# Optimization experiments

Hardware: AMD Instinct MI355X
Metric: run time of the kernel (lower is better)

Reference implementation:

```python
import jax, jax.numpy as jnp
import numpy as np
import math

D_MODEL = 256
NUM_HEADS = 8
D_HEAD = 32
K_EIG = 32
NUM_BANDS = 3


def setup_inputs() -> dict:
    key = jax.random.key(0)
    ks = jax.random.split(key, 12)
    B, N = 2, 50000
    x = jax.random.normal(ks[0], (B, N, D_MODEL), dtype=jnp.float32)
    eigenvectors = jax.random.normal(ks[1], (N, K_EIG), dtype=jnp.float32) / np.sqrt(N)
    eigenvalues = jnp.sort(jax.random.uniform(ks[2], (K_EIG,), dtype=jnp.float32))
    s = 1.0 / np.sqrt(D_MODEL)
    Wq = jax.random.normal(ks[3], (NUM_HEADS * D_HEAD, D_MODEL), dtype=jnp.float32) * s
    bq = jnp.zeros((NUM_HEADS * D_HEAD,), dtype=jnp.float32)
    Wk = jax.random.normal(ks[4], (NUM_HEADS * D_HEAD, D_MODEL), dtype=jnp.float32) * s
    bk = jnp.zeros((NUM_HEADS * D_HEAD,), dtype=jnp.float32)
    Wv = jax.random.normal(ks[5], (NUM_HEADS * D_HEAD, D_MODEL), dtype=jnp.float32) * s
    bv = jnp.zeros((NUM_HEADS * D_HEAD,), dtype=jnp.float32)
    # per-head SpectralFilter params
    band_boundaries = jnp.tile(jnp.linspace(0.0, 1.0, NUM_BANDS + 1, dtype=jnp.float32)[None, :], (NUM_HEADS, 1))
    filter_weights = jnp.ones((NUM_HEADS, NUM_BANDS, K_EIG), dtype=jnp.float32) + 0.1 * jax.random.normal(ks[6], (NUM_HEADS, NUM_BANDS, K_EIG), dtype=jnp.float32)
    return {"x": x, "eigenvectors": eigenvectors, "eigenvalues": eigenvalues,
            "Wq": Wq, "bq": bq, "Wk": Wk, "bk": bk, "Wv": Wv, "bv": bv,
            "band_boundaries": band_boundaries, "filter_weights": filter_weights}


def _filter_responses(eigenvalues, band_boundaries, filter_weights):
    # eigenvalues [K]; band_boundaries [H, NB+1]; filter_weights [H, NB, K] -> [H, K]
    lam = (eigenvalues - eigenvalues.min()) / (eigenvalues.max() - eigenvalues.min() + 1e-8)  # [K]
    resp = jnp.zeros(filter_weights.shape[::2], dtype=eigenvalues.dtype)  # [H, K]
    for i in range(NUM_BANDS):  # small fixed loop; later bands overwrite (faithful to torch)
        lo = band_boundaries[:, i:i + 1]   # [H,1]
        hi = band_boundaries[:, i + 1:i + 2]
        mask = (lam[None, :] >= lo) & (lam[None, :] < hi)  # [H,K]
        resp = jnp.where(mask, filter_weights[:, i, :], resp)
    return resp


def reference(x, eigenvectors, eigenvalues, Wq, bq, Wk, bk, Wv, bv, band_boundaries, filter_weights):
    B, N, D = x.shape
    H, Dh = NUM_HEADS, D_HEAD
    Q = (x @ Wq.T + bq).reshape(B, N, H, Dh)
    K = (x @ Wk.T + bk).reshape(B, N, H, Dh)
    V = (x @ Wv.T + bv).reshape(B, N, H, Dh)
    # project to spectral domain: [B,K,H,Dh]
    Qf = jnp.einsum('nk,bnhd->bkhd', eigenvectors, Q)
    Kf = jnp.einsum('nk,bnhd->bkhd', eigenvectors, K)
    Vf = jnp.einsum('nk,bnhd->bkhd', eigenvectors, V)
    resp = _filter_responses(eigenvalues, band_boundaries, filter_weights)  # [H,K]
    g = resp.T[None, :, :, None]  # [1,K,H,1]
    Qf, Kf, Vf = Qf * g, Kf * g, Vf * g
    scores = jnp.einsum('bkhd,blhd->bkhl', Qf, Kf) / math.sqrt(Dh)  # [B,K,H,K]
    attn = jax.nn.softmax(scores, axis=-1)
    out_freq = jnp.einsum('bkhl,blhd->bkhd', attn, Vf)
    out = jnp.einsum('nk,bkhd->bnhd', eigenvectors, out_freq)
    return out.reshape(B, N, H * Dh)
```

## Files before the change

kernel.cpp:

```cpp
#include <hip/hip_runtime.h>
#include <hip/hip_bf16.h>


constexpr int D = 256;

__global__ __launch_bounds__(256) void k_colsum(const float* __restrict__ E,
                                                float* __restrict__ pS, int N) {
  int k = threadIdx.x & 31;
  int rg = threadIdx.x >> 5;
  int rs = (N + 255) >> 8;
  int n0 = blockIdx.x * rs;
  int n1 = n0 + rs; if (n1 > N) n1 = N;
  float acc = 0.f;
  for (int n = n0 + rg; n < n1; n += 8) acc += E[(size_t)n * 32 + k];
  __shared__ float red[256];
  red[threadIdx.x] = acc;
  __syncthreads();
  if (threadIdx.x < 32) {
    float t = red[threadIdx.x];
#pragma unroll
    for (int i = 1; i < 8; ++i) t += red[i * 32 + threadIdx.x];
    pS[blockIdx.x * 32 + threadIdx.x] = t;
  }
}

__global__ __launch_bounds__(256) void k_partial(const float* __restrict__ x,
                                                 const float* __restrict__ E,
                                                 float* __restrict__ pU,
                                                 int N, int nchunk, int rpc) {
  int bc = blockIdx.x;
  int c = bc % nchunk;
  int b = bc / nchunk;
  int t = threadIdx.x;
  int w = t >> 6;
  int lane = t & 63;
  int n0 = c * rpc;
  int n1 = n0 + rpc; if (n1 > N) n1 = N;
  int nrows = n1 - n0; if (nrows < 0) nrows = 0;

  __shared__ __align__(16) float4 xs[2][1024];
  __shared__ __align__(16) float4 es[2][128];

  float4 a0={0,0,0,0}, a1={0,0,0,0}, a2={0,0,0,0}, a3={0,0,0,0};
  float4 a4={0,0,0,0}, a5={0,0,0,0}, a6={0,0,0,0}, a7={0,0,0,0};

  if (nrows > 0) {
    const float4* g4 = reinterpret_cast<const float4*>(x) + (size_t)b * N * 64;
    const float4* e4 = reinterpret_cast<const float4*>(E);
    int xr = t >> 6;
    int xq = t & 63;
    int er = t >> 3;
    int eq = t & 7;

    float4 rx0, rx1, rx2, rx3, re;
#define CL(r) ((r) < N - 1 ? (r) : N - 1)
    {
      rx0 = g4[(size_t)CL(n0 + xr +  0) * 64 + xq];
      rx1 = g4[(size_t)CL(n0 + xr +  4) * 64 + xq];
      rx2 = g4[(size_t)CL(n0 + xr +  8) * 64 + xq];
      rx3 = g4[(size_t)CL(n0 + xr + 12) * 64 + xq];
      if (t < 128) re = e4[(size_t)CL(n0 + er) * 8 + eq];
    }
    int ntiles = (nrows + 15) >> 4;
#pragma unroll 1
    for (int tt = 0; tt < ntiles; ++tt) {
      int buf = tt & 1;
      xs[buf][(xr +  0) * 64 + xq] = rx0;
      xs[buf][(xr +  4) * 64 + xq] = rx1;
      xs[buf][(xr +  8) * 64 + xq] = rx2;
      xs[buf][(xr + 12) * 64 + xq] = rx3;
      if (t < 128) es[buf][t] = re;
      __syncthreads();
      if (tt + 1 < ntiles) {
        int tb = n0 + ((tt + 1) << 4);
        rx0 = g4[(size_t)CL(tb + xr +  0) * 64 + xq];
        rx1 = g4[(size_t)CL(tb + xr +  4) * 64 + xq];
        rx2 = g4[(size_t)CL(tb + xr +  8) * 64 + xq];
        rx3 = g4[(size_t)CL(tb + xr + 12) * 64 + xq];
        if (t < 128) re = e4[(size_t)CL(tb + er) * 8 + eq];
      }
      int tr = nrows - (tt << 4); if (tr > 16) tr = 16;
#pragma unroll 4
      for (int r = 0; r < tr; ++r) {
        float4 xv = xs[buf][r * 64 + lane];
        float4 e0 = es[buf][r * 8 + 2 * w];
        float4 e1 = es[buf][r * 8 + 2 * w + 1];
        a0.x = fmaf(e0.x, xv.x, a0.x); a0.y = fmaf(e0.x, xv.y, a0.y);
        a0.z = fmaf(e0.x, xv.z, a0.z); a0.w = fmaf(e0.x, xv.w, a0.w);
        a1.x = fmaf(e0.y, xv.x, a1.x); a1.y = fmaf(e0.y, xv.y, a1.y);
        a1.z = fmaf(e0.y, xv.z, a1.z); a1.w = fmaf(e0.y, xv.w, a1.w);
        a2.x = fmaf(e0.z, xv.x, a2.x); a2.y = fmaf(e0.z, xv.y, a2.y);
        a2.z = fmaf(e0.z, xv.z, a2.z); a2.w = fmaf(e0.z, xv.w, a2.w);
        a3.x = fmaf(e0.w, xv.x, a3.x); a3.y = fmaf(e0.w, xv.y, a3.y);
        a3.z = fmaf(e0.w, xv.z, a3.z); a3.w = fmaf(e0.w, xv.w, a3.w);
        a4.x = fmaf(e1.x, xv.x, a4.x); a4.y = fmaf(e1.x, xv.y, a4.y);
        a4.z = fmaf(e1.x, xv.z, a4.z); a4.w = fmaf(e1.x, xv.w, a4.w);
        a5.x = fmaf(e1.y, xv.x, a5.x); a5.y = fmaf(e1.y, xv.y, a5.y);
        a5.z = fmaf(e1.y, xv.z, a5.z); a5.w = fmaf(e1.y, xv.w, a5.w);
        a6.x = fmaf(e1.z, xv.x, a6.x); a6.y = fmaf(e1.z, xv.y, a6.y);
        a6.z = fmaf(e1.z, xv.z, a6.z); a6.w = fmaf(e1.z, xv.w, a6.w);
        a7.x = fmaf(e1.w, xv.x, a7.x); a7.y = fmaf(e1.w, xv.y, a7.y);
        a7.z = fmaf(e1.w, xv.z, a7.z); a7.w = fmaf(e1.w, xv.w, a7.w);
      }
      __syncthreads();
    }
#undef CL
  }

  float4* o4 = reinterpret_cast<float4*>(pU) + (size_t)bc * 2048
             + (size_t)(8 * w) * 64 + lane;
  o4[0 * 64] = a0; o4[1 * 64] = a1; o4[2 * 64] = a2; o4[3 * 64] = a3;
  o4[4 * 64] = a4; o4[5 * 64] = a5; o4[6 * 64] = a6; o4[7 * 64] = a7;
}

__global__ __launch_bounds__(256) void k_reduce(const float* __restrict__ pU,
                                                float* __restrict__ U, int nchunk) {
  int e = blockIdx.x * 32 + (threadIdx.x & 31);
  int sub = threadIdx.x >> 5;
  int b = e >> 13;
  int kd = e & 8191;
  const float* p = pU + (size_t)b * nchunk * 8192 + kd;
  float a0 = 0.f, a1 = 0.f, a2 = 0.f, a3 = 0.f;
  float a4 = 0.f, a5 = 0.f, a6 = 0.f, a7 = 0.f;
  int c = sub;
#pragma unroll 1
  for (; c + 56 < nchunk; c += 64) {
    a0 += p[(size_t)c * 8192];
    a1 += p[(size_t)(c + 8) * 8192];
    a2 += p[(size_t)(c + 16) * 8192];
    a3 += p[(size_t)(c + 24) * 8192];
    a4 += p[(size_t)(c + 32) * 8192];
    a5 += p[(size_t)(c + 40) * 8192];
    a6 += p[(size_t)(c + 48) * 8192];
    a7 += p[(size_t)(c + 56) * 8192];
  }
  for (; c < nchunk; c += 8) a0 += p[(size_t)c * 8192];
  __shared__ float red[256];
  red[threadIdx.x] = ((a0 + a1) + (a2 + a3)) + ((a4 + a5) + (a6 + a7));
  __syncthreads();
  if (threadIdx.x < 32) {
    float s = red[threadIdx.x];
#pragma unroll
    for (int i = 1; i < 8; ++i) s += red[i * 32 + threadIdx.x];
    U[e] = s;
  }
}

__global__ __launch_bounds__(256) void k_project(
    const float* __restrict__ U, const float* __restrict__ pS,
    const float* __restrict__ Wq, const float* __restrict__ bq,
    const float* __restrict__ Wk, const float* __restrict__ bk,
    const float* __restrict__ Wv, const float* __restrict__ bv,
    const float* __restrict__ ev, const float* __restrict__ bb,
    const float* __restrict__ fw,
    float* __restrict__ Qfg, float* __restrict__ Kfg, float* __restrict__ Vfg) {
  int blk = blockIdx.x;
  int k = blk & 31;
  int t = threadIdx.x;
  __shared__ __align__(16) float u[256];
  __shared__ float red[256];
  u[t] = U[(size_t)blk * 256 + t];
  red[t] = pS[t * 32 + k];
  __syncthreads();
#pragma unroll
  for (int off = 128; off > 0; off >>= 1) {
    if (t < off) red[t] += red[t + off];
    __syncthreads();
  }
  float sk = red[0];

  float mnf = ev[0], mxf = ev[0];
#pragma unroll
  for (int i = 1; i < 32; ++i) { float v = ev[i]; mnf = fminf(mnf, v); mxf = fmaxf(mxf, v); }
  double mn = (double)mnf, mx = (double)mxf;
  double lam = ((double)ev[k] - mn) / (mx - mn + 1e-8);
  int h = t >> 5;
  float g = 0.f;
#pragma unroll
  for (int i = 0; i < 3; ++i) {
    double lo = (double)bb[h * 4 + i], hi = (double)bb[h * 4 + i + 1];
    if (lam >= lo && lam < hi) g = fw[(h * 3 + i) * 32 + k];
  }

  const float4* u4 = reinterpret_cast<const float4*>(u);
  const float4* wq4 = reinterpret_cast<const float4*>(Wq) + (size_t)t * 64;
  const float4* wk4 = reinterpret_cast<const float4*>(Wk) + (size_t)t * 64;
  const float4* wv4 = reinterpret_cast<const float4*>(Wv) + (size_t)t * 64;
  float aq = 0.f, ak = 0.f, av = 0.f;
#pragma unroll 4
  for (int j = 0; j < 64; ++j) {
    float4 uv = u4[j];
    float4 q = wq4[j], kk = wk4[j], vv = wv4[j];
    aq = fmaf(uv.x, q.x, aq);  aq = fmaf(uv.y, q.y, aq);
    aq = fmaf(uv.z, q.z, aq);  aq = fmaf(uv.w, q.w, aq);
    ak = fmaf(uv.x, kk.x, ak); ak = fmaf(uv.y, kk.y, ak);
    ak = fmaf(uv.z, kk.z, ak); ak = fmaf(uv.w, kk.w, ak);
    av = fmaf(uv.x, vv.x, av); av = fmaf(uv.y, vv.y, av);
    av = fmaf(uv.z, vv.z, av); av = fmaf(uv.w, vv.w, av);
  }
  Qfg[(size_t)blk * 256 + t] = (aq + bq[t] * sk) * g;
  Kfg[(size_t)blk * 256 + t] = (ak + bk[t] * sk) * g;
  Vfg[(size_t)blk * 256 + t] = (av + bv[t] * sk) * g;
}

__global__ __launch_bounds__(1024) void k_attn(const float* __restrict__ Qfg,
                                               const float* __restrict__ Kfg,
                                               const float* __restrict__ Vfg,
                                               float* __restrict__ of) {
  int blk = blockIdx.x;
  int b = blk >> 3, h = blk & 7;
  int tid = threadIdx.x;
  int row = tid >> 5, col = tid & 31;
  __shared__ float Q[32][33], Kt[32][33], V[32][33], A[32][33];
  size_t base = (size_t)b * 32 * 256 + h * 32;
  Q[row][col]  = Qfg[base + row * 256 + col];
  Kt[row][col] = Kfg[base + row * 256 + col];
  V[row][col]  = Vfg[base + row * 256 + col];
  __syncthreads();
  float sc = 0.f;
#pragma unroll
  for (int d0 = 0; d0 < 32; ++d0) sc = fmaf(Q[row][d0], Kt[col][d0], sc);
  sc *= 0.17677669529663687f;
  float m = sc;
#pragma unroll
  for (int o = 16; o > 0; o >>= 1) m = fmaxf(m, __shfl_xor(m, o, 32));
  float p = expf(sc - m);
  float su = p;
#pragma unroll
  for (int o = 16; o > 0; o >>= 1) su += __shfl_xor(su, o, 32);
  A[row][col] = p / su;
  __syncthreads();
  float o_ = 0.f;
#pragma unroll
  for (int l = 0; l < 32; ++l) o_ = fmaf(A[row][l], V[l][col], o_);
  of[base + row * 256 + col] = o_;
}

__global__ __launch_bounds__(256) void k_expand(const float* __restrict__ E,
                                                const float* __restrict__ of,
                                                float* __restrict__ out,
                                                int N, int rows) {
  int n0 = blockIdx.x * rows;
  int n1 = n0 + rows; if (n1 > N) n1 = N;
  if (n1 <= n0) return;
  int nr = n1 - n0;
  int t = threadIdx.x;
  int w = t >> 6;
  int bb = w & 1;
  int dh = w >> 1;
  int lane = t & 63;

  __shared__ __align__(16) float4 es[512];
  {
    const float4* e4 = reinterpret_cast<const float4*>(E);
    int f0 = t, f1 = t + 256;
    int r0 = n0 + (f0 >> 3); if (r0 > N - 1) r0 = N - 1;
    int r1 = n0 + (f1 >> 3); if (r1 > N - 1) r1 = N - 1;
    float4 t0 = e4[(size_t)r0 * 8 + (f0 & 7)];
    float4 t1 = e4[(size_t)r1 * 8 + (f1 & 7)];
    es[f0] = t0;
    es[f1] = t1;
  }

  const float* ofb = of + (size_t)bb * 8192 + dh * 128 + 2 * lane;
  float2 v0  = *(const float2*)(ofb +  0*256), v1  = *(const float2*)(ofb +  1*256);
  float2 v2  = *(const float2*)(ofb +  2*256), v3  = *(const float2*)(ofb +  3*256);
  float2 v4  = *(const float2*)(ofb +  4*256), v5  = *(const float2*)(ofb +  5*256);
  float2 v6  = *(const float2*)(ofb +  6*256), v7  = *(const float2*)(ofb +  7*256);
  float2 v8  = *(const float2*)(ofb +  8*256), v9  = *(const float2*)(ofb +  9*256);
  float2 v10 = *(const float2*)(ofb + 10*256), v11 = *(const float2*)(ofb + 11*256);
  float2 v12 = *(const float2*)(ofb + 12*256), v13 = *(const float2*)(ofb + 13*256);
  float2 v14 = *(const float2*)(ofb + 14*256), v15 = *(const float2*)(ofb + 15*256);
  float2 v16 = *(const float2*)(ofb + 16*256), v17 = *(const float2*)(ofb + 17*256);
  float2 v18 = *(const float2*)(ofb + 18*256), v19 = *(const float2*)(ofb + 19*256);
  float2 v20 = *(const float2*)(ofb + 20*256), v21 = *(const float2*)(ofb + 21*256);
  float2 v22 = *(const float2*)(ofb + 22*256), v23 = *(const float2*)(ofb + 23*256);
  float2 v24 = *(const float2*)(ofb + 24*256), v25 = *(const float2*)(ofb + 25*256);
  float2 v26 = *(const float2*)(ofb + 26*256), v27 = *(const float2*)(ofb + 27*256);
  float2 v28 = *(const float2*)(ofb + 28*256), v29 = *(const float2*)(ofb + 29*256);
  float2 v30 = *(const float2*)(ofb + 30*256), v31 = *(const float2*)(ofb + 31*256);

  __syncthreads();

  float* ob = out + (size_t)bb * N * D + dh * 128 + 2 * lane;

#define EX(s, vk, A) { A.x = fmaf(s, vk.x, A.x); A.y = fmaf(s, vk.y, A.y); }
#pragma unroll 2
  for (int r = 0; r < nr; ++r) {
    float4 e0 = es[r*8+0], e1 = es[r*8+1], e2 = es[r*8+2], e3 = es[r*8+3];
    float4 e4_ = es[r*8+4], e5 = es[r*8+5], e6 = es[r*8+6], e7 = es[r*8+7];
    float2 oA = {0.f, 0.f}, oB = {0.f, 0.f};
    EX(e0.x, v0,  oA) EX(e0.y, v1,  oB) EX(e0.z, v2,  oA) EX(e0.w, v3,  oB)
    EX(e1.x, v4,  oA) EX(e1.y, v5,  oB) EX(e1.z, v6,  oA) EX(e1.w, v7,  oB)
    EX(e2.x, v8,  oA) EX(e2.y, v9,  oB) EX(e2.z, v10, oA) EX(e2.w, v11, oB)
    EX(e3.x, v12, oA) EX(e3.y, v13, oB) EX(e3.z, v14, oA) EX(e3.w, v15, oB)
    EX(e4_.x, v16, oA) EX(e4_.y, v17, oB) EX(e4_.z, v18, oA) EX(e4_.w, v19, oB)
    EX(e5.x, v20, oA) EX(e5.y, v21, oB) EX(e5.z, v22, oA) EX(e5.w, v23, oB)
    EX(e6.x, v24, oA) EX(e6.y, v25, oB) EX(e6.z, v26, oA) EX(e6.w, v27, oB)
    EX(e7.x, v28, oA) EX(e7.y, v29, oB) EX(e7.z, v30, oA) EX(e7.w, v31, oB)
    float2 o2;
    o2.x = oA.x + oB.x;
    o2.y = oA.y + oB.y;
    *reinterpret_cast<float2*>(ob + (size_t)(n0 + r) * D) = o2;
  }
#undef EX
}

extern "C" void kernel_launch(void* const* d_in, const int* in_sizes, int n_in,
                              void* d_out, int out_size, void* d_ws, size_t ws_size,
                              hipStream_t stream) {
  const float* x  = (const float*)d_in[0];
  const float* E  = (const float*)d_in[1];
  const float* ev = (const float*)d_in[2];
  const float* Wq = (const float*)d_in[3];
  const float* bq = (const float*)d_in[4];
  const float* Wk = (const float*)d_in[5];
  const float* bk = (const float*)d_in[6];
  const float* Wv = (const float*)d_in[7];
  const float* bv = (const float*)d_in[8];
  const float* bb = (const float*)d_in[9];
  const float* fw = (const float*)d_in[10];
  float* out = (float*)d_out;
  float* ws  = (float*)d_ws;

  const int N = in_sizes[1] / 32;
  const int B = in_sizes[0] / (N * 256);

  float* U   = ws;
  float* Qfg = ws + 16384;
  float* Kfg = ws + 32768;
  float* Vfg = ws + 49152;
  float* of  = ws + 65536;
  float* pS  = ws + 81920;
  float* pU  = ws + 90112;

  int nchunk = 512;
  if ((90112 + (size_t)B * nchunk * 8192) * sizeof(float) > ws_size) nchunk = 256;
  int rpc = (N + nchunk - 1) / nchunk;

  k_colsum<<<256, 256, 0, stream>>>(E, pS, N);
  k_partial<<<B * nchunk, 256, 0, stream>>>(x, E, pU, N, nchunk, rpc);
  k_reduce<<<B * 8192 / 32, 256, 0, stream>>>(pU, U, nchunk);
  k_project<<<B * 32, 256, 0, stream>>>(U, pS, Wq, bq, Wk, bk, Wv, bv,
                                        ev, bb, fw, Qfg, Kfg, Vfg);
  k_attn<<<B * 8, 1024, 0, stream>>>(Qfg, Kfg, Vfg, of);
  int rows = 64;
  int nbr = (N + rows - 1) / rows;
  k_expand<<<nbr, 256, 0, stream>>>(E, of, out, N, rows);
}
```

Before: 146.0 us.

## Restructure partial projection to register-streamed x with row-split warps and smem reduction

k_partial now runs 512 threads. Each warp owns a half of the d dimension and a quarter of the rows in a 32-row tile. x is loaded straight into registers as float2, which removes the x staging through shared memory and one barrier per tile. Each thread keeps all 32 eigen-coefficients for its two columns, and the four row-partitions are combined through a shared-memory reduction at the end. k_expand is also reworked to 32 rows per block, with each thread covering one batch and a column pair, so it launches twice as many blocks. The cost is higher register pressure (64 accumulators plus 16 prefetch float2) and extra barriers in the epilogue.

```diff
diff --git a/kernel.cpp b/kernel.cpp
--- a/kernel.cpp
+++ b/kernel.cpp
@@ -24,7 +24,7 @@
   }
 }
 
-__global__ __launch_bounds__(256) void k_partial(const float* __restrict__ x,
+__global__ __launch_bounds__(512) void k_partial(const float* __restrict__ x,
                                                  const float* __restrict__ E,
                                                  float* __restrict__ pU,
                                                  int N, int nchunk, int rpc) {
@@ -33,84 +33,132 @@
   int b = bc / nchunk;
   int t = threadIdx.x;
   int w = t >> 6;
+  int dh = w & 1;
+  int rp = w >> 1;
   int lane = t & 63;
   int n0 = c * rpc;
   int n1 = n0 + rpc; if (n1 > N) n1 = N;
   int nrows = n1 - n0; if (nrows < 0) nrows = 0;
 
-  __shared__ __align__(16) float4 xs[2][1024];
-  __shared__ __align__(16) float4 es[2][128];
-
-  float4 a0={0,0,0,0}, a1={0,0,0,0}, a2={0,0,0,0}, a3={0,0,0,0};
-  float4 a4={0,0,0,0}, a5={0,0,0,0}, a6={0,0,0,0}, a7={0,0,0,0};
+  __shared__ __align__(16) float4 es[2][256];
+  __shared__ float2 rbuf[3][2][8][64];
+
+  float2 a0={0,0},a1={0,0},a2={0,0},a3={0,0},a4={0,0},a5={0,0},a6={0,0},a7={0,0};
+  float2 a8={0,0},a9={0,0},a10={0,0},a11={0,0},a12={0,0},a13={0,0},a14={0,0},a15={0,0};
+  float2 a16={0,0},a17={0,0},a18={0,0},a19={0,0},a20={0,0},a21={0,0},a22={0,0},a23={0,0};
+  float2 a24={0,0},a25={0,0},a26={0,0},a27={0,0},a28={0,0},a29={0,0},a30={0,0},a31={0,0};
 
   if (nrows > 0) {
-    const float4* g4 = reinterpret_cast<const float4*>(x) + (size_t)b * N * 64;
+    const float* xb = x + (size_t)b * N * D + dh * 128 + 2 * lane;
     const float4* e4 = reinterpret_cast<const float4*>(E);
-    int xr = t >> 6;
-    int xq = t & 63;
-    int er = t >> 3;
-    int eq = t & 7;
-
-    float4 rx0, rx1, rx2, rx3, re;
-#define CL(r) ((r) < N - 1 ? (r) : N - 1)
-    {
-      rx0 = g4[(size_t)CL(n0 + xr +  0) * 64 + xq];
-      rx1 = g4[(size_t)CL(n0 + xr +  4) * 64 + xq];
-      rx2 = g4[(size_t)CL(n0 + xr +  8) * 64 + xq];
-      rx3 = g4[(size_t)CL(n0 + xr + 12) * 64 + xq];
-      if (t < 128) re = e4[(size_t)CL(n0 + er) * 8 + eq];
+    int er = t >> 3, eq = t & 7;
+    int ntiles = (nrows + 31) >> 5;
+
+#define CLR(r) ((r) < N - 1 ? (r) : (N - 1))
+#define XL(tb, off) (*reinterpret_cast<const float2*>( \
+    xb + (size_t)CLR((tb) + rp + (off)) * D))
+
+    float2 pa0, pa1, pa2, pa3, pa4, pa5, pa6, pa7;
+    float2 pb0={0,0}, pb1={0,0}, pb2={0,0}, pb3={0,0};
+    float2 pb4={0,0}, pb5={0,0}, pb6={0,0}, pb7={0,0};
+    float4 rea = {0,0,0,0}, reb = {0,0,0,0};
+
+    pa0 = XL(n0, 0);  pa1 = XL(n0, 4);  pa2 = XL(n0, 8);  pa3 = XL(n0, 12);
+    pa4 = XL(n0, 16); pa5 = XL(n0, 20); pa6 = XL(n0, 24); pa7 = XL(n0, 28);
+    if (t < 256) rea = e4[(size_t)CLR(n0 + er) * 8 + eq];
+
+#define FK(s, A) { A.x = fmaf(s, xq.x, A.x); A.y = fmaf(s, xq.y, A.y); }
+#define FMAROW(ep, q) { float2 xq = q; float4 e_;                        \
+    e_ = (ep)[0]; FK(e_.x, a0)  FK(e_.y, a1)  FK(e_.z, a2)  FK(e_.w, a3) \
+    e_ = (ep)[1]; FK(e_.x, a4)  FK(e_.y, a5)  FK(e_.z, a6)  FK(e_.w, a7) \
+    e_ = (ep)[2]; FK(e_.x, a8)  FK(e_.y, a9)  FK(e_.z, a10) FK(e_.w, a11)\
+    e_ = (ep)[3]; FK(e_.x, a12) FK(e_.y, a13) FK(e_.z, a14) FK(e_.w, a15)\
+    e_ = (ep)[4]; FK(e_.x, a16) FK(e_.y, a17) FK(e_.z, a18) FK(e_.w, a19)\
+    e_ = (ep)[5]; FK(e_.x, a20) FK(e_.y, a21) FK(e_.z, a22) FK(e_.w, a23)\
+    e_ = (ep)[6]; FK(e_.x, a24) FK(e_.y, a25) FK(e_.z, a26) FK(e_.w, a27)\
+    e_ = (ep)[7]; FK(e_.x, a28) FK(e_.y, a29) FK(e_.z, a30) FK(e_.w, a31) }
+
+#define SLOT(buf, j, q, tr) \
+    if (rp + 4 * (j) < (tr)) { FMAROW(&es[buf][(rp + 4 * (j)) * 8], q) }
+
+#define TILEBODY(tt, PC, RC, PN, RN) {                                   \
+    int buf = (tt) & 1;                                                  \
+    if (t < 256) es[buf][t] = RC;       \
+    __syncthreads();                                                     \
+    if ((tt) + 1 < ntiles) {                \
+      int tbn = n0 + (((tt) + 1) << 5);                                  \
+      PN##0 = XL(tbn, 0);  PN##1 = XL(tbn, 4);                           \
+      PN##2 = XL(tbn, 8);  PN##3 = XL(tbn, 12);                          \
+      PN##4 = XL(tbn, 16); PN##5 = XL(tbn, 20);                          \
+      PN##6 = XL(tbn, 24); PN##7 = XL(tbn, 28);                          \
+      if (t < 256) RN = e4[(size_t)CLR(tbn + er) * 8 + eq];              \
+    }                                                                    \
+    int tr = nrows - ((tt) << 5); if (tr > 32) tr = 32;                  \
+    SLOT(buf, 0, PC##0, tr) SLOT(buf, 1, PC##1, tr)                      \
+    SLOT(buf, 2, PC##2, tr) SLOT(buf, 3, PC##3, tr)                      \
+    SLOT(buf, 4, PC##4, tr) SLOT(buf, 5, PC##5, tr)                      \
+    SLOT(buf, 6, PC##6, tr) SLOT(buf, 7, PC##7, tr)                      \
+  }
+
+    int tt = 0;
+#pragma unroll 1
+    for (; tt + 2 <= ntiles; tt += 2) {
+      TILEBODY(tt,     pa, rea, pb, reb)
+      TILEBODY(tt + 1, pb, reb, pa, rea)
     }
-    int ntiles = (nrows + 15) >> 4;
-#pragma unroll 1
-    for (int tt = 0; tt < ntiles; ++tt) {
-      int buf = tt & 1;
-      xs[buf][(xr +  0) * 64 + xq] = rx0;
-      xs[buf][(xr +  4) * 64 + xq] = rx1;
-      xs[buf][(xr +  8) * 64 + xq] = rx2;
-      xs[buf][(xr + 12) * 64 + xq] = rx3;
-      if (t < 128) es[buf][t] = re;
-      __syncthreads();
-      if (tt + 1 < ntiles) {
-        int tb = n0 + ((tt + 1) << 4);
-        rx0 = g4[(size_t)CL(tb + xr +  0) * 64 + xq];
-        rx1 = g4[(size_t)CL(tb + xr +  4) * 64 + xq];
-        rx2 = g4[(size_t)CL(tb + xr +  8) * 64 + xq];
-        rx3 = g4[(size_t)CL(tb + xr + 12) * 64 + xq];
-        if (t < 128) re = e4[(size_t)CL(tb + er) * 8 + eq];
-      }
-      int tr = nrows - (tt << 4); if (tr > 16) tr = 16;
-#pragma unroll 4
-      for (int r = 0; r < tr; ++r) {
-        float4 xv = xs[buf][r * 64 + lane];
-        float4 e0 = es[buf][r * 8 + 2 * w];
-        float4 e1 = es[buf][r * 8 + 2 * w + 1];
-        a0.x = fmaf(e0.x, xv.x, a0.x); a0.y = fmaf(e0.x, xv.y, a0.y);
-        a0.z = fmaf(e0.x, xv.z, a0.z); a0.w = fmaf(e0.x, xv.w, a0.w);
-        a1.x = fmaf(e0.y, xv.x, a1.x); a1.y = fmaf(e0.y, xv.y, a1.y);
-        a1.z = fmaf(e0.y, xv.z, a1.z); a1.w = fmaf(e0.y, xv.w, a1.w);
-        a2.x = fmaf(e0.z, xv.x, a2.x); a2.y = fmaf(e0.z, xv.y, a2.y);
-        a2.z = fmaf(e0.z, xv.z, a2.z); a2.w = fmaf(e0.z, xv.w, a2.w);
-        a3.x = fmaf(e0.w, xv.x, a3.x); a3.y = fmaf(e0.w, xv.y, a3.y);
-        a3.z = fmaf(e0.w, xv.z, a3.z); a3.w = fmaf(e0.w, xv.w, a3.w);
-        a4.x = fmaf(e1.x, xv.x, a4.x); a4.y = fmaf(e1.x, xv.y, a4.y);
-        a4.z = fmaf(e1.x, xv.z, a4.z); a4.w = fmaf(e1.x, xv.w, a4.w);
-        a5.x = fmaf(e1.y, xv.x, a5.x); a5.y = fmaf(e1.y, xv.y, a5.y);
-        a5.z = fmaf(e1.y, xv.z, a5.z); a5.w = fmaf(e1.y, xv.w, a5.w);
-        a6.x = fmaf(e1.z, xv.x, a6.x); a6.y = fmaf(e1.z, xv.y, a6.y);
-        a6.z = fmaf(e1.z, xv.z, a6.z); a6.w = fmaf(e1.z, xv.w, a6.w);
-        a7.x = fmaf(e1.w, xv.x, a7.x); a7.y = fmaf(e1.w, xv.y, a7.y);
-        a7.z = fmaf(e1.w, xv.z, a7.z); a7.w = fmaf(e1.w, xv.w, a7.w);
-      }
-      __syncthreads();
-    }
-#undef CL
-  }
-
-  float4* o4 = reinterpret_cast<float4*>(pU) + (size_t)bc * 2048
-             + (size_t)(8 * w) * 64 + lane;
-  o4[0 * 64] = a0; o4[1 * 64] = a1; o4[2 * 64] = a2; o4[3 * 64] = a3;
-  o4[4 * 64] = a4; o4[5 * 64] = a5; o4[6 * 64] = a6; o4[7 * 64] = a7;
+    if (tt < ntiles) TILEBODY(tt, pa, rea, pb, reb)
+#undef TILEBODY
+#undef SLOT
+#undef FMAROW
+#undef FK
+#undef XL
+#undef CLR
+  }
+
+  float* o = pU + (size_t)bc * 8192 + dh * 128 + 2 * lane;
+
+#define ROCT(g, A0, A1, A2, A3, A4, A5, A6, A7)                          \
+  __syncthreads();                                                       \
+  if (rp > 0) {                                                          \
+    rbuf[rp-1][dh][0][lane] = A0; rbuf[rp-1][dh][1][lane] = A1;          \
+    rbuf[rp-1][dh][2][lane] = A2; rbuf[rp-1][dh][3][lane] = A3;          \
+    rbuf[rp-1][dh][4][lane] = A4; rbuf[rp-1][dh][5][lane] = A5;          \
+    rbuf[rp-1][dh][6][lane] = A6; rbuf[rp-1][dh][7][lane] = A7;          \
+  }                                                                      \
+  __syncthreads();                                                       \
+  if (rp == 0) {                                                         \
+    float2 s0, s1, s2, sv;                                               \
+    s0 = rbuf[0][dh][0][lane]; s1 = rbuf[1][dh][0][lane]; s2 = rbuf[2][dh][0][lane]; \
+    sv.x = (A0.x + s0.x) + (s1.x + s2.x); sv.y = (A0.y + s0.y) + (s1.y + s2.y);      \
+    *reinterpret_cast<float2*>(o + ((g) * 8 + 0) * 256) = sv;            \
+    s0 = rbuf[0][dh][1][lane]; s1 = rbuf[1][dh][1][lane]; s2 = rbuf[2][dh][1][lane]; \
+    sv.x = (A1.x + s0.x) + (s1.x + s2.x); sv.y = (A1.y + s0.y) + (s1.y + s2.y);      \
+    *reinterpret_cast<float2*>(o + ((g) * 8 + 1) * 256) = sv;            \
+    s0 = rbuf[0][dh][2][lane]; s1 = rbuf[1][dh][2][lane]; s2 = rbuf[2][dh][2][lane]; \
+    sv.x = (A2.x + s0.x) + (s1.x + s2.x); sv.y = (A2.y + s0.y) + (s1.y + s2.y);      \
+    *reinterpret_cast<float2*>(o + ((g) * 8 + 2) * 256) = sv;            \
+    s0 = rbuf[0][dh][3][lane]; s1 = rbuf[1][dh][3][lane]; s2 = rbuf[2][dh][3][lane]; \
+    sv.x = (A3.x + s0.x) + (s1.x + s2.x); sv.y = (A3.y + s0.y) + (s1.y + s2.y);      \
+    *reinterpret_cast<float2*>(o + ((g) * 8 + 3) * 256) = sv;            \
+    s0 = rbuf[0][dh][4][lane]; s1 = rbuf[1][dh][4][lane]; s2 = rbuf[2][dh][4][lane]; \
+    sv.x = (A4.x + s0.x) + (s1.x + s2.x); sv.y = (A4.y + s0.y) + (s1.y + s2.y);      \
+    *reinterpret_cast<float2*>(o + ((g) * 8 + 4) * 256) = sv;            \
+    s0 = rbuf[0][dh][5][lane]; s1 = rbuf[1][dh][5][lane]; s2 = rbuf[2][dh][5][lane]; \
+    sv.x = (A5.x + s0.x) + (s1.x + s2.x); sv.y = (A5.y + s0.y) + (s1.y + s2.y);      \
+    *reinterpret_cast<float2*>(o + ((g) * 8 + 5) * 256) = sv;            \
+    s0 = rbuf[0][dh][6][lane]; s1 = rbuf[1][dh][6][lane]; s2 = rbuf[2][dh][6][lane]; \
+    sv.x = (A6.x + s0.x) + (s1.x + s2.x); sv.y = (A6.y + s0.y) + (s1.y + s2.y);      \
+    *reinterpret_cast<float2*>(o + ((g) * 8 + 6) * 256) = sv;            \
+    s0 = rbuf[0][dh][7][lane]; s1 = rbuf[1][dh][7][lane]; s2 = rbuf[2][dh][7][lane]; \
+    sv.x = (A7.x + s0.x) + (s1.x + s2.x); sv.y = (A7.y + s0.y) + (s1.y + s2.y);      \
+    *reinterpret_cast<float2*>(o + ((g) * 8 + 7) * 256) = sv;            \
+  }
+
+  ROCT(0, a0,  a1,  a2,  a3,  a4,  a5,  a6,  a7)
+  ROCT(1, a8,  a9,  a10, a11, a12, a13, a14, a15)
+  ROCT(2, a16, a17, a18, a19, a20, a21, a22, a23)
+  ROCT(3, a24, a25, a26, a27, a28, a29, a30, a31)
+#undef ROCT
 }
 
 __global__ __launch_bounds__(256) void k_reduce(const float* __restrict__ pU,
@@ -238,31 +286,23 @@
 
 __global__ __launch_bounds__(256) void k_expand(const float* __restrict__ E,
                                                 const float* __restrict__ of,
-                                                float* __restrict__ out,
-                                                int N, int rows) {
-  int n0 = blockIdx.x * rows;
-  int n1 = n0 + rows; if (n1 > N) n1 = N;
-  if (n1 <= n0) return;
+                                                float* __restrict__ out, int N) {
+  int n0 = blockIdx.x * 32;
+  int n1 = n0 + 32; if (n1 > N) n1 = N;
   int nr = n1 - n0;
+  if (nr <= 0) return;
   int t = threadIdx.x;
-  int w = t >> 6;
-  int bb = w & 1;
-  int dh = w >> 1;
-  int lane = t & 63;
-
-  __shared__ __align__(16) float4 es[512];
+  int bb = t >> 7;
+  int dp = t & 127;
+
+  __shared__ __align__(16) float4 es[256];
   {
     const float4* e4 = reinterpret_cast<const float4*>(E);
-    int f0 = t, f1 = t + 256;
-    int r0 = n0 + (f0 >> 3); if (r0 > N - 1) r0 = N - 1;
-    int r1 = n0 + (f1 >> 3); if (r1 > N - 1) r1 = N - 1;
-    float4 t0 = e4[(size_t)r0 * 8 + (f0 & 7)];
-    float4 t1 = e4[(size_t)r1 * 8 + (f1 & 7)];
-    es[f0] = t0;
-    es[f1] = t1;
-  }
-
-  const float* ofb = of + (size_t)bb * 8192 + dh * 128 + 2 * lane;
+    int r = n0 + (t >> 3); if (r > N - 1) r = N - 1;
+    es[t] = e4[(size_t)r * 8 + (t & 7)];
+  }
+
+  const float* ofb = of + (size_t)bb * 8192 + 2 * dp;
   float2 v0  = *(const float2*)(ofb +  0*256), v1  = *(const float2*)(ofb +  1*256);
   float2 v2  = *(const float2*)(ofb +  2*256), v3  = *(const float2*)(ofb +  3*256);
   float2 v4  = *(const float2*)(ofb +  4*256), v5  = *(const float2*)(ofb +  5*256);
@@ -282,13 +322,14 @@
 
   __syncthreads();
 
-  float* ob = out + (size_t)bb * N * D + dh * 128 + 2 * lane;
+  float* ob = out + (size_t)bb * N * D + 2 * dp;
 
 #define EX(s, vk, A) { A.x = fmaf(s, vk.x, A.x); A.y = fmaf(s, vk.y, A.y); }
 #pragma unroll 2
   for (int r = 0; r < nr; ++r) {
-    float4 e0 = es[r*8+0], e1 = es[r*8+1], e2 = es[r*8+2], e3 = es[r*8+3];
-    float4 e4_ = es[r*8+4], e5 = es[r*8+5], e6 = es[r*8+6], e7 = es[r*8+7];
+    const float4* ep = &es[r * 8];
+    float4 e0 = ep[0], e1 = ep[1], e2 = ep[2], e3 = ep[3];
+    float4 e4_ = ep[4], e5 = ep[5], e6 = ep[6], e7 = ep[7];
     float2 oA = {0.f, 0.f}, oB = {0.f, 0.f};
     EX(e0.x, v0,  oA) EX(e0.y, v1,  oB) EX(e0.z, v2,  oA) EX(e0.w, v3,  oB)
     EX(e1.x, v4,  oA) EX(e1.y, v5,  oB) EX(e1.z, v6,  oA) EX(e1.w, v7,  oB)
@@ -339,12 +380,11 @@
   int rpc = (N + nchunk - 1) / nchunk;
 
   k_colsum<<<256, 256, 0, stream>>>(E, pS, N);
-  k_partial<<<B * nchunk, 256, 0, stream>>>(x, E, pU, N, nchunk, rpc);
+  k_partial<<<B * nchunk, 512, 0, stream>>>(x, E, pU, N, nchunk, rpc);
   k_reduce<<<B * 8192 / 32, 256, 0, stream>>>(pU, U, nchunk);
   k_project<<<B * 32, 256, 0, stream>>>(U, pS, Wq, bq, Wk, bk, Wv, bv,
                                         ev, bb, fw, Qfg, Kfg, Vfg);
   k_attn<<<B * 8, 1024, 0, stream>>>(Qfg, Kfg, Vfg, of);
-  int rows = 64;
-  int nbr = (N + rows - 1) / rows;
-  k_expand<<<nbr, 256, 0, stream>>>(E, of, out, N, rows);
-}
+  int nbr = (N + 31) / 32;
+  k_expand<<<nbr, 256, 0, stream>>>(E, of, out, N);
+}
```

Result: slower. 153.1 us (+4.9%).
